# Kernel optimization log

Measured on AMD Instinct MI355X. Metric: run time of the kernel, lower is better.

The kernel has to match this reference:

```python
import jax, jax.numpy as jnp
import numpy as np

B, H, W, C = 512, 128, 128, 4


def setup_inputs() -> dict:
    key = jax.random.key(0)
    # One-hot gridworld observation: mostly empty (ch 0), sparse food (ch 1),
    # self (ch 2), opponent (ch 3).  ~1/40 chance per special channel per cell,
    # so with H*W=16384 cells every batch has food and an opponent w.h.p.
    cat = jax.random.randint(key, (B, H, W), 0, 40)
    channel = jnp.where(cat == 1, 1, jnp.where(cat == 2, 2, jnp.where(cat == 3, 3, 0)))
    x = jax.nn.one_hot(channel, C, dtype=jnp.float32)
    return {"x": x}


def reference(x):
    # Faithful vectorization of the per-batch Python loop:
    #   food cells = x[...,1]==1 ; first opponent cell (row-major) = x[...,3]==1
    #   if >1 food and opp != [3,6]: target = food cell nearest to opp (first argmin)
    #   elif exactly 1 food: target = that cell
    #   else (>1 food, opp == [3,6]): target = (0,0)
    #   write 1.0 into g_map at target iff any food exists.
    Bs, Hs, Ws, _ = x.shape
    rr, cc = jnp.meshgrid(jnp.arange(Hs), jnp.arange(Ws), indexing="ij")  # [H,W]

    food = x[..., 1] == 1.0                     # [B,H,W]
    opp = (x[..., 3] == 1.0).reshape(Bs, -1)    # [B,H*W]
    # first opponent index in row-major order (torch nonzero()[0])
    opp_first = jnp.argmax(opp, axis=1)         # [B]
    opp_r = (opp_first // Ws).astype(jnp.float32)
    opp_c = (opp_first % Ws).astype(jnp.float32)

    dr = rr[None].astype(jnp.float32) - opp_r[:, None, None]
    dc = cc[None].astype(jnp.float32) - opp_c[:, None, None]
    dist = jnp.sqrt(dr * dr + dc * dc)          # [B,H,W]

    BIG = jnp.float32(1e30)
    masked = jnp.where(food, dist, BIG).reshape(Bs, -1)
    min_idx = jnp.argmin(masked, axis=1)        # first min => matches torch.argmin over row-major food list

    food_count = food.reshape(Bs, -1).sum(axis=1)
    opp_at_start = (opp_r == 3.0) & (opp_c == 6.0)  # opp_start = [3,6]

    use_min = (food_count == 1) | ((food_count > 1) & ~opp_at_start)
    tgt = jnp.where(use_min, min_idx, 0)        # else target_coords = (0,0)
    write = (food_count > 0).astype(x.dtype)

    g_flat = jnp.zeros((Bs, Hs * Ws), dtype=x.dtype)
    g_flat = g_flat.at[jnp.arange(Bs), tgt].set(write)  # setting 0.0 is a no-op on zeros
    g_map = g_flat.reshape(Bs, Hs, Ws)
    return (g_map, jnp.zeros_like(g_map))
```

## Files before the change

### kernel.cpp

```cpp
#include <hip/hip_runtime.h>


#define HW_CELLS 16384
#define W_DIM    128

__global__ __launch_bounds__(512)
void oracle_kernel(const float4* __restrict__ x,
                   float* __restrict__ out0,
                   float* __restrict__ out1) {
    const int b   = blockIdx.x;
    const int tid = threadIdx.x;

    __shared__ unsigned int foodmask[HW_CELLS / 32];
    __shared__ unsigned int opp_min;
    __shared__ unsigned int key_min;
    __shared__ unsigned int food_cnt;

    foodmask[tid] = 0u;
    if (tid == 0) {
        opp_min  = 0xFFFFFFFFu;
        key_min  = 0xFFFFFFFFu;
        food_cnt = 0u;
    }
    __syncthreads();

    const float4* xb = x + (size_t)b * HW_CELLS;

    for (int i = 0; i < HW_CELLS / 512; ++i) {
        const int cell = tid + i * 512;
        const float4 v = xb[cell];
        if (v.y == 1.0f) atomicOr(&foodmask[cell >> 5], 1u << (cell & 31));
        if (v.w == 1.0f) atomicMin(&opp_min, (unsigned)cell);
    }

    float4* o0 = reinterpret_cast<float4*>(out0 + (size_t)b * HW_CELLS);
    float4* o1 = reinterpret_cast<float4*>(out1 + (size_t)b * HW_CELLS);
    const float4 z = make_float4(0.f, 0.f, 0.f, 0.f);
    for (int i = 0; i < HW_CELLS / 4 / 512; ++i) {
        o0[tid + i * 512] = z;
        o1[tid + i * 512] = z;
    }

    __syncthreads();

    unsigned opp = opp_min;
    if (opp == 0xFFFFFFFFu) opp = 0u;
    const int opp_r = (int)(opp >> 7);
    const int opp_c = (int)(opp & (W_DIM - 1));

    unsigned m   = foodmask[tid];
    const int cnt = __popc(m);
    unsigned local_key = 0xFFFFFFFFu;
    while (m) {
        const int bit = __ffs(m) - 1;
        m &= m - 1u;
        const int idx = (tid << 5) | bit;
        const int r = idx >> 7;
        const int c = idx & (W_DIM - 1);
        const int dr = r - opp_r;
        const int dc = c - opp_c;
        const unsigned sq = (unsigned)(dr * dr + dc * dc);
        const unsigned key = (sq << 14) | (unsigned)idx;
        if (key < local_key) local_key = key;
    }
    if (local_key != 0xFFFFFFFFu) atomicMin(&key_min, local_key);
    if (cnt) atomicAdd(&food_cnt, (unsigned)cnt);

    __syncthreads();

    if (tid == 0) {
        const unsigned fc = food_cnt;
        if (fc > 0u) {
            const unsigned min_idx = key_min & 16383u;
            const bool opp_at_start = (opp_r == 3) && (opp_c == 6);
            const bool use_min = (fc == 1u) || (fc > 1u && !opp_at_start);
            const unsigned tgt = use_min ? min_idx : 0u;
            out0[(size_t)b * HW_CELLS + tgt] = 1.0f;
        }
    }
}

extern "C" void kernel_launch(void* const* d_in, const int* in_sizes, int n_in,
                              void* d_out, int out_size, void* d_ws, size_t ws_size,
                              hipStream_t stream) {
    const float4* x = (const float4*)d_in[0];
    float* out = (float*)d_out;
    const int B = 512;
    float* out0 = out;
    float* out1 = out + (size_t)B * HW_CELLS;

    oracle_kernel<<<B, 512, 0, stream>>>(x, out0, out1);
}
```

Baseline: 34.07 us.

## Split into scan kernel writing targets and separate full-grid output fill kernel

The fused per-batch kernel is split in two. The first kernel only scans the input and records a target index per batch in workspace. The second, fully parallel kernel writes both output tensors as zeros and places the single 1.0 by checking the stored target. This removes the zero-fill stores from the scan blocks and spreads output writes over many small blocks, at the cost of a second launch and a serial dependency between the two kernels.

```diff
diff --git a/kernel.cpp b/kernel.cpp
--- a/kernel.cpp
+++ b/kernel.cpp
@@ -3,11 +3,10 @@
 
 #define HW_CELLS 16384
 #define W_DIM    128
+#define B_DIM    512
 
 __global__ __launch_bounds__(512)
-void oracle_kernel(const float4* __restrict__ x,
-                   float* __restrict__ out0,
-                   float* __restrict__ out1) {
+void scan_kernel(const float4* __restrict__ x, unsigned* __restrict__ tgt) {
     const int b   = blockIdx.x;
     const int tid = threadIdx.x;
 
@@ -32,15 +31,6 @@
         if (v.y == 1.0f) atomicOr(&foodmask[cell >> 5], 1u << (cell & 31));
         if (v.w == 1.0f) atomicMin(&opp_min, (unsigned)cell);
     }
-
-    float4* o0 = reinterpret_cast<float4*>(out0 + (size_t)b * HW_CELLS);
-    float4* o1 = reinterpret_cast<float4*>(out1 + (size_t)b * HW_CELLS);
-    const float4 z = make_float4(0.f, 0.f, 0.f, 0.f);
-    for (int i = 0; i < HW_CELLS / 4 / 512; ++i) {
-        o0[tid + i * 512] = z;
-        o1[tid + i * 512] = z;
-    }
-
     __syncthreads();
 
     unsigned opp = opp_min;
@@ -70,13 +60,32 @@
 
     if (tid == 0) {
         const unsigned fc = food_cnt;
+        unsigned t = 0xFFFFFFFFu;
         if (fc > 0u) {
             const unsigned min_idx = key_min & 16383u;
             const bool opp_at_start = (opp_r == 3) && (opp_c == 6);
             const bool use_min = (fc == 1u) || (fc > 1u && !opp_at_start);
-            const unsigned tgt = use_min ? min_idx : 0u;
-            out0[(size_t)b * HW_CELLS + tgt] = 1.0f;
+            t = use_min ? min_idx : 0u;
         }
+        tgt[b] = t;
+    }
+}
+
+__global__ __launch_bounds__(256)
+void fill_kernel(float4* __restrict__ out, const unsigned* __restrict__ tgt) {
+    const int f = blockIdx.x * 256 + threadIdx.x;
+    #pragma unroll
+    for (int i = 0; i < 4; ++i) {
+        const int idx = f + i * (4096 * 256);
+        float4 v = make_float4(0.f, 0.f, 0.f, 0.f);
+        if (i < 2) {
+            const unsigned b = (unsigned)idx >> 12;
+            const unsigned t = tgt[b];
+            if ((t >> 2) == ((unsigned)idx & 4095u)) {
+                reinterpret_cast<float*>(&v)[t & 3u] = 1.0f;
+            }
+        }
+        out[idx] = v;
     }
 }
 
@@ -84,10 +93,9 @@
                               void* d_out, int out_size, void* d_ws, size_t ws_size,
                               hipStream_t stream) {
     const float4* x = (const float4*)d_in[0];
-    float* out = (float*)d_out;
-    const int B = 512;
-    float* out0 = out;
-    float* out1 = out + (size_t)B * HW_CELLS;
+    float4* out = (float4*)d_out;
+    unsigned* tgt = (unsigned*)d_ws;
 
-    oracle_kernel<<<B, 512, 0, stream>>>(x, out0, out1);
+    scan_kernel<<<B_DIM, 512, 0, stream>>>(x, tgt);
+    fill_kernel<<<4096, 256, 0, stream>>>(out, tgt);
 }
```

After: 60.47 us. 1.77x slower.
